# Kernel optimization log

Hardware: AMD Instinct MI355X
Metric: run time of the kernel (lower is better)

The kernel has to match this reference:

```python
import jax, jax.numpy as jnp
import numpy as np

B, NREG, C, H = 1024, 16, 128, 256
N = B * NREG          # batched graph nodes
E = 131072            # GCN edges
NE = NREG * NREG      # OD-pair edges (must equal nregion^2)


def setup_inputs() -> dict:
    key = jax.random.key(0)
    ks = jax.random.split(key, 12)
    state = jax.random.normal(ks[0], (N, C), dtype=jnp.float32)
    edge_index = jax.random.randint(ks[1], (2, E), 0, N, dtype=jnp.int64)
    action = jax.random.uniform(ks[2], (B, NREG, NREG), dtype=jnp.float32)
    edges = jax.random.randint(ks[3], (NE, 2), 0, NREG, dtype=jnp.int64)
    s = 1.0 / np.sqrt(C)
    Wc = jax.random.uniform(ks[4], (C, C), jnp.float32, -s, s)
    bc = jax.random.uniform(ks[5], (C,), jnp.float32, -s, s)
    s1 = 1.0 / np.sqrt(2 * C + 1)
    W1 = jax.random.uniform(ks[6], (2 * C + 1, H), jnp.float32, -s1, s1)
    b1 = jax.random.uniform(ks[7], (H,), jnp.float32, -s1, s1)
    s2 = 1.0 / np.sqrt(H)
    W2 = jax.random.uniform(ks[8], (H, H), jnp.float32, -s2, s2)
    b2 = jax.random.uniform(ks[9], (H,), jnp.float32, -s2, s2)
    W3 = jax.random.uniform(ks[10], (H, 1), jnp.float32, -s2, s2)
    b3 = jax.random.uniform(ks[11], (1,), jnp.float32, -s2, s2)
    return {"state": state, "edge_index": edge_index, "action": action,
            "edges": edges, "Wc": Wc, "bc": bc, "W1": W1, "b1": b1,
            "W2": W2, "b2": b2, "W3": W3, "b3": b3}


def gcn_conv(x, edge_index, Wc, bc):
    n = x.shape[0]
    loop = jnp.arange(n, dtype=edge_index.dtype)
    src = jnp.concatenate([edge_index[0], loop])
    dst = jnp.concatenate([edge_index[1], loop])
    deg = jax.ops.segment_sum(jnp.ones_like(dst, dtype=x.dtype), dst, num_segments=n)
    dinv = jnp.where(deg > 0, jax.lax.rsqrt(deg), 0.0)
    norm = dinv[src] * dinv[dst]               # [E+N]
    xw = x @ Wc                                 # [N, C]
    msg = xw[src] * norm[:, None]
    agg = jax.ops.segment_sum(msg, dst, num_segments=n)
    return agg + bc


def reference(state, edge_index, action, edges, Wc, bc, W1, b1, W2, b2, W3, b3):
    out = jax.nn.relu(gcn_conv(state, edge_index, Wc, bc))
    x = (out + state).reshape(B, NREG, C)
    ef = jnp.concatenate([x[:, edges[:, 0], :], x[:, edges[:, 1], :]], axis=2)  # [B, NE, 2C]
    a = action.reshape(B, NE, 1)
    cat = jnp.concatenate([ef, a], axis=-1)     # [B, NE, 2C+1]
    h = jax.nn.relu(cat @ W1 + b1)
    h = jax.nn.relu(h @ W2 + b2)
    h = jnp.sum(h, axis=1)                      # [B, H]
    return (h @ W3 + b3).squeeze(-1)            # [B]
```

## Files before the change

kernel.cpp:

```cpp
#include <hip/hip_runtime.h>
#include <hip/hip_bf16.h>

#define NB    1024
#define NRG   16
#define NC    128
#define NH    256
#define NNODE (NB*NRG)
#define NEDGE 131072
#define NEP   256

typedef __attribute__((ext_vector_type(8))) short short8;
typedef __attribute__((ext_vector_type(4))) float f32x4;

__device__ __forceinline__ unsigned short f2bf(float f) {
    union { float f; unsigned int u; } x; x.f = f;
    unsigned int u = x.u + 0x7fffu + ((x.u >> 16) & 1u);
    return (unsigned short)(u >> 16);
}


__global__ void cast_bf16_kernel(const float* __restrict__ in,
                                 unsigned short* __restrict__ out, int n) {
    int i = blockIdx.x * 256 + threadIdx.x;
    if (i < n) out[i] = f2bf(in[i]);
}

__global__ void transpose_bf16_kernel(const float* __restrict__ W,
                                      unsigned short* __restrict__ WT, int R, int C) {
    int c = blockIdx.x, r = threadIdx.x;
    WT[c * R + r] = f2bf(W[r * C + c]);
}

__global__ void prep_w1t_kernel(const float* __restrict__ W1,
                                unsigned short* __restrict__ WT) {
    int j = blockIdx.x, k = threadIdx.x;
    float v = (j < NH) ? W1[k * NH + j] : W1[(128 + k) * NH + (j - NH)];
    WT[j * 128 + k] = f2bf(v);
}


__global__ void deg_kernel(const int* __restrict__ ei, int* __restrict__ deg) {
    int e = blockIdx.x * 256 + threadIdx.x;
    if (e < NEDGE) atomicAdd(&deg[ei[NEDGE + e] & (NNODE - 1)], 1);
}

__global__ void scan_kernel(const int* __restrict__ deg, int* __restrict__ off,
                            float* __restrict__ dinv) {
    __shared__ int sums[1024];
    int t = threadIdx.x;
    int base = t * 16;
    int local[16];
    int s = 0;
    #pragma unroll
    for (int j = 0; j < 16; j++) { local[j] = deg[base + j]; s += local[j]; }
    sums[t] = s;
    __syncthreads();
    int v = s;
    for (int o = 1; o < 1024; o <<= 1) {
        int u = (t >= o) ? sums[t - o] : 0;
        __syncthreads();
        v += u; sums[t] = v;
        __syncthreads();
    }
    int run = v - s;
    #pragma unroll
    for (int j = 0; j < 16; j++) { off[base + j] = run; run += local[j]; }
    #pragma unroll
    for (int j = 0; j < 16; j++)
        dinv[base + j] = rsqrtf((float)(local[j] + 1));
}

__global__ void scatter_kernel(const int* __restrict__ ei, const int* __restrict__ off,
                               int* __restrict__ cursor, int* __restrict__ csr) {
    int e = blockIdx.x * 256 + threadIdx.x;
    if (e < NEDGE) {
        int d = ei[NEDGE + e] & (NNODE - 1);
        int p = atomicAdd(&cursor[d], 1);
        csr[off[d] + p] = ei[e] & (NNODE - 1);
    }
}

__global__ __launch_bounds__(128) void gather_kernel(
    const float* __restrict__ xw, const int* __restrict__ csr,
    const int* __restrict__ off, const int* __restrict__ deg,
    const float* __restrict__ dinv, const float* __restrict__ bc,
    const float* __restrict__ state, unsigned short* __restrict__ xb) {
    int n = blockIdx.x, ch = threadIdx.x;
    float dn = dinv[n];
    float acc = xw[(size_t)n * NC + ch] * dn;
    int st = off[n], d = deg[n];
    for (int i = 0; i < d; i++) {
        int s = csr[st + i];
        acc += xw[(size_t)s * NC + ch] * dinv[s];
    }
    acc *= dn;
    float o = acc + bc[ch];
    o = o > 0.f ? o : 0.f;
    xb[(size_t)n * NC + ch] = f2bf(o + state[(size_t)n * NC + ch]);
}

__global__ __launch_bounds__(256) void gemm_bf16_k128(
    const unsigned short* __restrict__ A, const unsigned short* __restrict__ BT,
    float* __restrict__ D, int N, const float* __restrict__ bias, int biasLim) {
    __shared__ unsigned short As[64 * 128];
    __shared__ unsigned short Bs[64 * 128];
    const int m0 = blockIdx.x << 6, n0 = blockIdx.y << 6;
    const int t = threadIdx.x, lane = t & 63, w = t >> 6;
    {
        const int r = t >> 2, seg = t & 3;
        const uint4* ga = (const uint4*)(A + ((size_t)(m0 + r) << 7) + (seg << 5));
        const uint4* gb = (const uint4*)(BT + ((size_t)(n0 + r) << 7) + (seg << 5));
        uint4 a0 = ga[0], a1 = ga[1], a2 = ga[2], a3 = ga[3];
        uint4 c0 = gb[0], c1 = gb[1], c2 = gb[2], c3 = gb[3];
        char* ap = (char*)As + r * 256;
        char* bp = (char*)Bs + r * 256;
        int cb = seg << 6, sw = (r & 7) << 4;
        *(uint4*)(ap + ((cb +  0) ^ sw)) = a0;
        *(uint4*)(ap + ((cb + 16) ^ sw)) = a1;
        *(uint4*)(ap + ((cb + 32) ^ sw)) = a2;
        *(uint4*)(ap + ((cb + 48) ^ sw)) = a3;
        *(uint4*)(bp + ((cb +  0) ^ sw)) = c0;
        *(uint4*)(bp + ((cb + 16) ^ sw)) = c1;
        *(uint4*)(bp + ((cb + 32) ^ sw)) = c2;
        *(uint4*)(bp + ((cb + 48) ^ sw)) = c3;
    }
    __syncthreads();
    f32x4 acc[4];
    #pragma unroll
    for (int n = 0; n < 4; n++) acc[n] = (f32x4){0.f, 0.f, 0.f, 0.f};
    const int arow = (w << 4) + (lane & 15);
    const int asw = (arow & 7) << 4;
    #pragma unroll
    for (int s = 0; s < 4; s++) {
        short8 af = *(const short8*)((const char*)As + arow * 256 +
                                     (((s << 6) + ((lane >> 4) << 4)) ^ asw));
        #pragma unroll
        for (int n = 0; n < 4; n++) {
            int brow = (n << 4) + (lane & 15);
            short8 bf = *(const short8*)((const char*)Bs + brow * 256 +
                         (((s << 6) + ((lane >> 4) << 4)) ^ ((brow & 7) << 4)));
            acc[n] = __builtin_amdgcn_mfma_f32_16x16x32_bf16(af, bf, acc[n], 0, 0, 0);
        }
    }
    #pragma unroll
    for (int n = 0; n < 4; n++) {
        int col = n0 + (n << 4) + (lane & 15);
        float bv = 0.f;
        if (bias != nullptr && col < biasLim) bv = bias[col];
        #pragma unroll
        for (int r = 0; r < 4; r++) {
            int row = m0 + (w << 4) + ((lane >> 4) << 2) + r;
            D[(size_t)row * N + col] = acc[n][r] + bv;
        }
    }
}

__global__ __launch_bounds__(256) void fused_kernel(
    const float* __restrict__ UV, const unsigned short* __restrict__ W2T,
    const int* __restrict__ edges, const float* __restrict__ action,
    const float* __restrict__ W1, const float* __restrict__ b2,
    const float* __restrict__ W3, const float* __restrict__ b3,
    float* __restrict__ out) {
    __shared__ unsigned short h1s[64 * 256];
    __shared__ int srcL[NEP], dstL[NEP];
    __shared__ float aL[NEP], w1cL[NH], b2L[NH], w3L[NH];
    __shared__ float red[4];
    const int b = blockIdx.x;
    const int t = threadIdx.x;
    const int lane = t & 63;
    const int w = t >> 6;
    srcL[t] = edges[2 * t] & (NRG - 1);
    dstL[t] = edges[2 * t + 1] & (NRG - 1);
    aL[t]   = action[(size_t)b * NEP + t];
    w1cL[t] = W1[256 * NH + t];
    b2L[t]  = b2[t];
    w3L[t]  = W3[t];
    __syncthreads();

    const int kO = t & 31;
    const int eS = t >> 5;
    float partial = 0.f;

    for (int c = 0; c < 4; ++c) {
        #pragma unroll
        for (int it = 0; it < 8; ++it) {
            int el = (it << 3) + eS;
            int e  = (c << 6) + el;
            int sn = srcL[e], dn = dstL[e];
            float ae = aL[e];
            const float* up = UV + (((size_t)b * NRG + sn) << 9) + (kO << 3);
            const float* vp = UV + (((size_t)b * NRG + dn) << 9) + NH + (kO << 3);
            float4 u0 = *(const float4*)up;
            float4 u1 = *(const float4*)(up + 4);
            float4 v0 = *(const float4*)vp;
            float4 v1 = *(const float4*)(vp + 4);
            float4 c0 = *(const float4*)(w1cL + (kO << 3));
            float4 c1 = *(const float4*)(w1cL + (kO << 3) + 4);
            union { unsigned short us[8]; uint4 q; } P;
            float y;
            y = u0.x + v0.x + ae * c0.x; P.us[0] = f2bf(y > 0.f ? y : 0.f);
            y = u0.y + v0.y + ae * c0.y; P.us[1] = f2bf(y > 0.f ? y : 0.f);
            y = u0.z + v0.z + ae * c0.z; P.us[2] = f2bf(y > 0.f ? y : 0.f);
            y = u0.w + v0.w + ae * c0.w; P.us[3] = f2bf(y > 0.f ? y : 0.f);
            y = u1.x + v1.x + ae * c1.x; P.us[4] = f2bf(y > 0.f ? y : 0.f);
            y = u1.y + v1.y + ae * c1.y; P.us[5] = f2bf(y > 0.f ? y : 0.f);
            y = u1.z + v1.z + ae * c1.z; P.us[6] = f2bf(y > 0.f ? y : 0.f);
            y = u1.w + v1.w + ae * c1.w; P.us[7] = f2bf(y > 0.f ? y : 0.f);
            *(uint4*)((char*)h1s + el * 512 + ((kO << 4) ^ ((el & 7) << 4))) = P.q;
        }
        __syncthreads();
        f32x4 acc[4][4];
        #pragma unroll
        for (int m = 0; m < 4; m++)
            #pragma unroll
            for (int n = 0; n < 4; n++) acc[m][n] = (f32x4){0.f, 0.f, 0.f, 0.f};
        for (int s = 0; s < 8; ++s) {
            short8 af[4], bf[4];
            #pragma unroll
            for (int m = 0; m < 4; m++) {
                int row = (m << 4) + (lane & 15);
                af[m] = *(const short8*)((const char*)h1s + row * 512 +
                          (((s << 6) + ((lane >> 4) << 4)) ^ ((row & 7) << 4)));
            }
            #pragma unroll
            for (int n = 0; n < 4; n++) {
                int col = (w << 6) + (n << 4) + (lane & 15);
                bf[n] = *(const short8*)(W2T + (size_t)col * NH + (s << 5) +
                                         ((lane >> 4) << 3));
            }
            #pragma unroll
            for (int m = 0; m < 4; m++)
                #pragma unroll
                for (int n = 0; n < 4; n++)
                    acc[m][n] = __builtin_amdgcn_mfma_f32_16x16x32_bf16(
                                    af[m], bf[n], acc[m][n], 0, 0, 0);
        }
        #pragma unroll
        for (int n = 0; n < 4; n++) {
            int col = (w << 6) + (n << 4) + (lane & 15);
            float bb = b2L[col], ww = w3L[col];
            #pragma unroll
            for (int m = 0; m < 4; m++)
                #pragma unroll
                for (int r = 0; r < 4; r++) {
                    float v = acc[m][n][r] + bb;
                    partial += (v > 0.f ? v : 0.f) * ww;
                }
        }
        __syncthreads();
    }
    #pragma unroll
    for (int o = 32; o; o >>= 1) partial += __shfl_down(partial, o, 64);
    if (lane == 0) red[w] = partial;
    __syncthreads();
    if (t == 0) out[b] = red[0] + red[1] + red[2] + red[3] + b3[0];
}


extern "C" void kernel_launch(void* const* d_in, const int* in_sizes, int n_in,
                              void* d_out, int out_size, void* d_ws, size_t ws_size,
                              hipStream_t stream) {
    const float* state  = (const float*)d_in[0];
    const int*   ei     = (const int*)d_in[1];
    const float* action = (const float*)d_in[2];
    const int*   edges  = (const int*)d_in[3];
    const float* Wc     = (const float*)d_in[4];
    const float* bc     = (const float*)d_in[5];
    const float* W1     = (const float*)d_in[6];
    const float* b1     = (const float*)d_in[7];
    const float* W2     = (const float*)d_in[8];
    const float* b2     = (const float*)d_in[9];
    const float* W3     = (const float*)d_in[10];
    const float* b3     = (const float*)d_in[11];
    float* out = (float*)d_out;

    if (ws_size < 38830080u) return;

    char* ws = (char*)d_ws;
    unsigned short* stateB = (unsigned short*)(ws + 0);
    unsigned short* xB     = (unsigned short*)(ws + 0);
    float*          xw     = (float*)(ws + 4194304);
    float*          UV     = (float*)(ws + 4194304);
    unsigned short* WcT    = (unsigned short*)(ws + 37748736);
    unsigned short* W1T    = (unsigned short*)(ws + 37781504);
    unsigned short* W2T    = (unsigned short*)(ws + 37912576);
    int*            deg    = (int*)(ws + 38043648);
    int*            offs   = (int*)(ws + 38109184);
    int*            cursor = (int*)(ws + 38174720);
    float*          dinv   = (float*)(ws + 38240256);
    int*            csr    = (int*)(ws + 38305792);

    hipMemsetAsync(deg, 0, NNODE * sizeof(int), stream);
    hipMemsetAsync(cursor, 0, NNODE * sizeof(int), stream);

    cast_bf16_kernel<<<(NNODE * NC) / 256, 256, 0, stream>>>(state, stateB, NNODE * NC);
    transpose_bf16_kernel<<<128, 128, 0, stream>>>(Wc, WcT, 128, 128);
    prep_w1t_kernel<<<512, 128, 0, stream>>>(W1, W1T);
    transpose_bf16_kernel<<<256, 256, 0, stream>>>(W2, W2T, 256, 256);

    deg_kernel<<<NEDGE / 256, 256, 0, stream>>>(ei, deg);
    scan_kernel<<<1, 1024, 0, stream>>>(deg, offs, dinv);
    scatter_kernel<<<NEDGE / 256, 256, 0, stream>>>(ei, offs, cursor, csr);

    gemm_bf16_k128<<<dim3(NNODE / 64, 2), 256, 0, stream>>>(stateB, WcT, xw, 128,
                                                            nullptr, 0);
    gather_kernel<<<NNODE, 128, 0, stream>>>(xw, csr, offs, deg, dinv, bc, state, xB);
    gemm_bf16_k128<<<dim3(NNODE / 64, 8), 256, 0, stream>>>(xB, W1T, UV, 512, b1, NH);

    fused_kernel<<<NB, 256, 0, stream>>>(UV, W2T, edges, action, W1, b2, W3, b3, out);
}
```

Measured before the change: 230.6 us.

## Merge prep kernels, parallelize CSR offsets, fold dinv into GEMM, restructure MLP

The cast, transpose and degree-count kernels are merged into one launch, and the two memsets become one. The single-block scan is replaced by wave-level prefix sums that claim global offsets with an atomic, so CSR segments land in arbitrary but disjoint order. The source-side dinv scaling moves into the first GEMM epilogue as a row scale, and the gather stages neighbor indices in shared memory. The fused MLP kernel now processes its output columns in two halves to cut accumulator registers (launch bounds 4) and hoists the W1 column loads. Fewer launches and higher occupancy are traded for nondeterministic CSR order, which can change the order of floating-point sums.

After: 317.8 us. 1.38x slower.

```diff
diff --git a/kernel.cpp b/kernel.cpp
--- a/kernel.cpp
+++ b/kernel.cpp
@@ -18,56 +18,53 @@
     return (unsigned short)(u >> 16);
 }
 
-
-__global__ void cast_bf16_kernel(const float* __restrict__ in,
-                                 unsigned short* __restrict__ out, int n) {
-    int i = blockIdx.x * 256 + threadIdx.x;
-    if (i < n) out[i] = f2bf(in[i]);
-}
-
-__global__ void transpose_bf16_kernel(const float* __restrict__ W,
-                                      unsigned short* __restrict__ WT, int R, int C) {
-    int c = blockIdx.x, r = threadIdx.x;
-    WT[c * R + r] = f2bf(W[r * C + c]);
-}
-
-__global__ void prep_w1t_kernel(const float* __restrict__ W1,
-                                unsigned short* __restrict__ WT) {
-    int j = blockIdx.x, k = threadIdx.x;
-    float v = (j < NH) ? W1[k * NH + j] : W1[(128 + k) * NH + (j - NH)];
-    WT[j * 128 + k] = f2bf(v);
-}
-
-
-__global__ void deg_kernel(const int* __restrict__ ei, int* __restrict__ deg) {
-    int e = blockIdx.x * 256 + threadIdx.x;
-    if (e < NEDGE) atomicAdd(&deg[ei[NEDGE + e] & (NNODE - 1)], 1);
-}
-
-__global__ void scan_kernel(const int* __restrict__ deg, int* __restrict__ off,
-                            float* __restrict__ dinv) {
-    __shared__ int sums[1024];
-    int t = threadIdx.x;
-    int base = t * 16;
-    int local[16];
-    int s = 0;
-    #pragma unroll
-    for (int j = 0; j < 16; j++) { local[j] = deg[base + j]; s += local[j]; }
-    sums[t] = s;
-    __syncthreads();
-    int v = s;
-    for (int o = 1; o < 1024; o <<= 1) {
-        int u = (t >= o) ? sums[t - o] : 0;
-        __syncthreads();
-        v += u; sums[t] = v;
-        __syncthreads();
-    }
-    int run = v - s;
-    #pragma unroll
-    for (int j = 0; j < 16; j++) { off[base + j] = run; run += local[j]; }
-    #pragma unroll
-    for (int j = 0; j < 16; j++)
-        dinv[base + j] = rsqrtf((float)(local[j] + 1));
+__global__ void prep_kernel(const float* __restrict__ state, unsigned short* __restrict__ stateB,
+                            const float* __restrict__ Wc, unsigned short* __restrict__ WcT,
+                            const float* __restrict__ W1, unsigned short* __restrict__ W1T,
+                            const float* __restrict__ W2, unsigned short* __restrict__ W2T,
+                            const int* __restrict__ ei, int* __restrict__ deg) {
+    int b = blockIdx.x, t = threadIdx.x;
+    if (b < 8192) { int i = b * 256 + t; stateB[i] = f2bf(state[i]); return; }
+    b -= 8192;
+    if (b < 64) {
+        int i = b * 256 + t; int r = i & 127, c = i >> 7;
+        WcT[c * 128 + r] = f2bf(Wc[r * 128 + c]); return;
+    }
+    b -= 64;
+    if (b < 256) {
+        int i = b * 256 + t; int k = i & 127, j = i >> 7;
+        float v = (j < NH) ? W1[k * NH + j] : W1[(128 + k) * NH + (j - NH)];
+        W1T[j * 128 + k] = f2bf(v); return;
+    }
+    b -= 256;
+    if (b < 256) {
+        int i = b * 256 + t; int r = i & 255, c = i >> 8;
+        W2T[c * 256 + r] = f2bf(W2[r * 256 + c]); return;
+    }
+    b -= 256;
+    {
+        int e = b * 256 + t;
+        if (e < NEDGE) atomicAdd(&deg[ei[NEDGE + e] & (NNODE - 1)], 1);
+    }
+}
+
+
+__global__ void offs_kernel(const int* __restrict__ deg, int* __restrict__ off,
+                            float* __restrict__ dinv, int* __restrict__ gctr) {
+    int n = blockIdx.x * 256 + threadIdx.x;
+    int lane = threadIdx.x & 63;
+    int d = deg[n];
+    int s = d;
+    #pragma unroll
+    for (int o = 1; o < 64; o <<= 1) {
+        int u = __shfl_up(s, o, 64);
+        if (lane >= o) s += u;
+    }
+    int base = 0;
+    if (lane == 63) base = atomicAdd(gctr, s);
+    base = __shfl(base, 63, 64);
+    off[n] = base + s - d;
+    dinv[n] = rsqrtf((float)(d + 1));
 }
 
 __global__ void scatter_kernel(const int* __restrict__ ei, const int* __restrict__ off,
@@ -81,27 +78,32 @@
 }
 
 __global__ __launch_bounds__(128) void gather_kernel(
-    const float* __restrict__ xw, const int* __restrict__ csr,
+    const float* __restrict__ y, const int* __restrict__ csr,
     const int* __restrict__ off, const int* __restrict__ deg,
     const float* __restrict__ dinv, const float* __restrict__ bc,
     const float* __restrict__ state, unsigned short* __restrict__ xb) {
+    __shared__ int nb[32];
     int n = blockIdx.x, ch = threadIdx.x;
-    float dn = dinv[n];
-    float acc = xw[(size_t)n * NC + ch] * dn;
     int st = off[n], d = deg[n];
-    for (int i = 0; i < d; i++) {
-        int s = csr[st + i];
-        acc += xw[(size_t)s * NC + ch] * dinv[s];
-    }
-    acc *= dn;
-    float o = acc + bc[ch];
-    o = o > 0.f ? o : 0.f;
-    xb[(size_t)n * NC + ch] = f2bf(o + state[(size_t)n * NC + ch]);
+    float acc = y[(size_t)n * NC + ch];
+    for (int base = 0; base < d; base += 32) {
+        int cnt = min(d - base, 32);
+        if (ch < cnt) nb[ch] = csr[st + base + ch];
+        __syncthreads();
+        #pragma unroll 4
+        for (int i = 0; i < cnt; i++)
+            acc += y[(size_t)nb[i] * NC + ch];
+        __syncthreads();
+    }
+    acc *= dinv[n];
+    float o = fmaxf(acc + bc[ch], 0.f) + state[(size_t)n * NC + ch];
+    xb[(size_t)n * NC + ch] = f2bf(o);
 }
 
 __global__ __launch_bounds__(256) void gemm_bf16_k128(
     const unsigned short* __restrict__ A, const unsigned short* __restrict__ BT,
-    float* __restrict__ D, int N, const float* __restrict__ bias, int biasLim) {
+    float* __restrict__ D, int N, const float* __restrict__ bias, int biasLim,
+    const float* __restrict__ rowscale) {
     __shared__ unsigned short As[64 * 128];
     __shared__ unsigned short Bs[64 * 128];
     const int m0 = blockIdx.x << 6, n0 = blockIdx.y << 6;
@@ -142,20 +144,22 @@
             acc[n] = __builtin_amdgcn_mfma_f32_16x16x32_bf16(af, bf, acc[n], 0, 0, 0);
         }
     }
+    const int rb = m0 + (w << 4) + ((lane >> 4) << 2);
+    float sc[4];
+    #pragma unroll
+    for (int r = 0; r < 4; r++) sc[r] = rowscale ? rowscale[rb + r] : 1.f;
     #pragma unroll
     for (int n = 0; n < 4; n++) {
         int col = n0 + (n << 4) + (lane & 15);
         float bv = 0.f;
         if (bias != nullptr && col < biasLim) bv = bias[col];
         #pragma unroll
-        for (int r = 0; r < 4; r++) {
-            int row = m0 + (w << 4) + ((lane >> 4) << 2) + r;
-            D[(size_t)row * N + col] = acc[n][r] + bv;
-        }
-    }
-}
-
-__global__ __launch_bounds__(256) void fused_kernel(
+        for (int r = 0; r < 4; r++)
+            D[(size_t)(rb + r) * N + col] = acc[n][r] * sc[r] + bv;
+    }
+}
+
+__global__ __launch_bounds__(256, 4) void fused_kernel(
     const float* __restrict__ UV, const unsigned short* __restrict__ W2T,
     const int* __restrict__ edges, const float* __restrict__ action,
     const float* __restrict__ W1, const float* __restrict__ b2,
@@ -179,73 +183,74 @@
 
     const int kO = t & 31;
     const int eS = t >> 5;
+    const float4 wc0 = *(const float4*)(w1cL + (kO << 3));
+    const float4 wc1 = *(const float4*)(w1cL + (kO << 3) + 4);
+    const float* UVb = UV + ((size_t)b * NRG << 9);
     float partial = 0.f;
 
     for (int c = 0; c < 4; ++c) {
-        #pragma unroll
+        #pragma unroll 4
         for (int it = 0; it < 8; ++it) {
             int el = (it << 3) + eS;
             int e  = (c << 6) + el;
             int sn = srcL[e], dn = dstL[e];
             float ae = aL[e];
-            const float* up = UV + (((size_t)b * NRG + sn) << 9) + (kO << 3);
-            const float* vp = UV + (((size_t)b * NRG + dn) << 9) + NH + (kO << 3);
+            const float* up = UVb + (sn << 9) + (kO << 3);
+            const float* vp = UVb + (dn << 9) + NH + (kO << 3);
             float4 u0 = *(const float4*)up;
             float4 u1 = *(const float4*)(up + 4);
             float4 v0 = *(const float4*)vp;
             float4 v1 = *(const float4*)(vp + 4);
-            float4 c0 = *(const float4*)(w1cL + (kO << 3));
-            float4 c1 = *(const float4*)(w1cL + (kO << 3) + 4);
             union { unsigned short us[8]; uint4 q; } P;
             float y;
-            y = u0.x + v0.x + ae * c0.x; P.us[0] = f2bf(y > 0.f ? y : 0.f);
-            y = u0.y + v0.y + ae * c0.y; P.us[1] = f2bf(y > 0.f ? y : 0.f);
-            y = u0.z + v0.z + ae * c0.z; P.us[2] = f2bf(y > 0.f ? y : 0.f);
-            y = u0.w + v0.w + ae * c0.w; P.us[3] = f2bf(y > 0.f ? y : 0.f);
-            y = u1.x + v1.x + ae * c1.x; P.us[4] = f2bf(y > 0.f ? y : 0.f);
-            y = u1.y + v1.y + ae * c1.y; P.us[5] = f2bf(y > 0.f ? y : 0.f);
-            y = u1.z + v1.z + ae * c1.z; P.us[6] = f2bf(y > 0.f ? y : 0.f);
-            y = u1.w + v1.w + ae * c1.w; P.us[7] = f2bf(y > 0.f ? y : 0.f);
+            y = u0.x + v0.x + ae * wc0.x; P.us[0] = f2bf(fmaxf(y, 0.f));
+            y = u0.y + v0.y + ae * wc0.y; P.us[1] = f2bf(fmaxf(y, 0.f));
+            y = u0.z + v0.z + ae * wc0.z; P.us[2] = f2bf(fmaxf(y, 0.f));
+            y = u0.w + v0.w + ae * wc0.w; P.us[3] = f2bf(fmaxf(y, 0.f));
+            y = u1.x + v1.x + ae * wc1.x; P.us[4] = f2bf(fmaxf(y, 0.f));
+            y = u1.y + v1.y + ae * wc1.y; P.us[5] = f2bf(fmaxf(y, 0.f));
+            y = u1.z + v1.z + ae * wc1.z; P.us[6] = f2bf(fmaxf(y, 0.f));
+            y = u1.w + v1.w + ae * wc1.w; P.us[7] = f2bf(fmaxf(y, 0.f));
             *(uint4*)((char*)h1s + el * 512 + ((kO << 4) ^ ((el & 7) << 4))) = P.q;
         }
         __syncthreads();
-        f32x4 acc[4][4];
         #pragma unroll
-        for (int m = 0; m < 4; m++)
-            #pragma unroll
-            for (int n = 0; n < 4; n++) acc[m][n] = (f32x4){0.f, 0.f, 0.f, 0.f};
-        for (int s = 0; s < 8; ++s) {
-            short8 af[4], bf[4];
-            #pragma unroll
-            for (int m = 0; m < 4; m++) {
-                int row = (m << 4) + (lane & 15);
-                af[m] = *(const short8*)((const char*)h1s + row * 512 +
-                          (((s << 6) + ((lane >> 4) << 4)) ^ ((row & 7) << 4)));
-            }
-            #pragma unroll
-            for (int n = 0; n < 4; n++) {
-                int col = (w << 6) + (n << 4) + (lane & 15);
-                bf[n] = *(const short8*)(W2T + (size_t)col * NH + (s << 5) +
-                                         ((lane >> 4) << 3));
-            }
+        for (int nh = 0; nh < 2; ++nh) {
+            f32x4 acc[4][2];
             #pragma unroll
             for (int m = 0; m < 4; m++)
                 #pragma unroll
-                for (int n = 0; n < 4; n++)
-                    acc[m][n] = __builtin_amdgcn_mfma_f32_16x16x32_bf16(
-                                    af[m], bf[n], acc[m][n], 0, 0, 0);
-        }
-        #pragma unroll
-        for (int n = 0; n < 4; n++) {
-            int col = (w << 6) + (n << 4) + (lane & 15);
-            float bb = b2L[col], ww = w3L[col];
+                for (int n = 0; n < 2; n++) acc[m][n] = (f32x4){0.f, 0.f, 0.f, 0.f};
             #pragma unroll
-            for (int m = 0; m < 4; m++)
+            for (int s = 0; s < 8; ++s) {
+                short8 af[4];
                 #pragma unroll
-                for (int r = 0; r < 4; r++) {
-                    float v = acc[m][n][r] + bb;
-                    partial += (v > 0.f ? v : 0.f) * ww;
+                for (int m = 0; m < 4; m++) {
+                    int row = (m << 4) + (lane & 15);
+                    af[m] = *(const short8*)((const char*)h1s + row * 512 +
+                              (((s << 6) + ((lane >> 4) << 4)) ^ ((row & 7) << 4)));
                 }
+                #pragma unroll
+                for (int n = 0; n < 2; n++) {
+                    int col = (w << 6) + (nh << 5) + (n << 4) + (lane & 15);
+                    short8 bf = *(const short8*)(W2T + (size_t)col * NH + (s << 5) +
+                                                 ((lane >> 4) << 3));
+                    #pragma unroll
+                    for (int m = 0; m < 4; m++)
+                        acc[m][n] = __builtin_amdgcn_mfma_f32_16x16x32_bf16(
+                                        af[m], bf, acc[m][n], 0, 0, 0);
+                }
+            }
+            #pragma unroll
+            for (int n = 0; n < 2; n++) {
+                int col = (w << 6) + (nh << 5) + (n << 4) + (lane & 15);
+                float bb = b2L[col], ww = w3L[col];
+                #pragma unroll
+                for (int m = 0; m < 4; m++)
+                    #pragma unroll
+                    for (int r = 0; r < 4; r++)
+                        partial += fmaxf(acc[m][n][r] + bb, 0.f) * ww;
+            }
         }
         __syncthreads();
     }
@@ -279,33 +284,31 @@
     char* ws = (char*)d_ws;
     unsigned short* stateB = (unsigned short*)(ws + 0);
     unsigned short* xB     = (unsigned short*)(ws + 0);
-    float*          xw     = (float*)(ws + 4194304);
+    float*          y      = (float*)(ws + 4194304);
     float*          UV     = (float*)(ws + 4194304);
     unsigned short* WcT    = (unsigned short*)(ws + 37748736);
     unsigned short* W1T    = (unsigned short*)(ws + 37781504);
     unsigned short* W2T    = (unsigned short*)(ws + 37912576);
     int*            deg    = (int*)(ws + 38043648);
-    int*            offs   = (int*)(ws + 38109184);
-    int*            cursor = (int*)(ws + 38174720);
-    float*          dinv   = (float*)(ws + 38240256);
-    int*            csr    = (int*)(ws + 38305792);
-
-    hipMemsetAsync(deg, 0, NNODE * sizeof(int), stream);
-    hipMemsetAsync(cursor, 0, NNODE * sizeof(int), stream);
-
-    cast_bf16_kernel<<<(NNODE * NC) / 256, 256, 0, stream>>>(state, stateB, NNODE * NC);
-    transpose_bf16_kernel<<<128, 128, 0, stream>>>(Wc, WcT, 128, 128);
-    prep_w1t_kernel<<<512, 128, 0, stream>>>(W1, W1T);
-    transpose_bf16_kernel<<<256, 256, 0, stream>>>(W2, W2T, 256, 256);
-
-    deg_kernel<<<NEDGE / 256, 256, 0, stream>>>(ei, deg);
-    scan_kernel<<<1, 1024, 0, stream>>>(deg, offs, dinv);
+    int*            cursor = (int*)(ws + 38109184);
+    int*            csr    = (int*)(ws + 38174720);
+    int*            gctr   = (int*)(ws + 38174720);
+    int*            offs   = (int*)(ws + 38699008);
+    float*          dinv   = (float*)(ws + 38764544);
+
+    hipMemsetAsync(ws + 38043648, 0, 131076, stream);
+
+    prep_kernel<<<9280, 256, 0, stream>>>(state, stateB, Wc, WcT, W1, W1T, W2, W2T,
+                                          ei, deg);
+
+    offs_kernel<<<NNODE / 256, 256, 0, stream>>>(deg, offs, dinv, gctr);
     scatter_kernel<<<NEDGE / 256, 256, 0, stream>>>(ei, offs, cursor, csr);
 
-    gemm_bf16_k128<<<dim3(NNODE / 64, 2), 256, 0, stream>>>(stateB, WcT, xw, 128,
-                                                            nullptr, 0);
-    gather_kernel<<<NNODE, 128, 0, stream>>>(xw, csr, offs, deg, dinv, bc, state, xB);
-    gemm_bf16_k128<<<dim3(NNODE / 64, 8), 256, 0, stream>>>(xB, W1T, UV, 512, b1, NH);
+    gemm_bf16_k128<<<dim3(NNODE / 64, 2), 256, 0, stream>>>(stateB, WcT, y, 128,
+                                                            nullptr, 0, dinv);
+    gather_kernel<<<NNODE, 128, 0, stream>>>(y, csr, offs, deg, dinv, bc, state, xB);
+    gemm_bf16_k128<<<dim3(NNODE / 64, 8), 256, 0, stream>>>(xB, W1T, UV, 512, b1, NH,
+                                                            nullptr);
 
     fused_kernel<<<NB, 256, 0, stream>>>(UV, W2T, edges, action, W1, b2, W3, b3, out);
 }
```
